# Kernel tuning notes

Measured on AMD Instinct MI355X. Metric: run time of the kernel, lower is better.

The kernel has to match this reference:

```python
import jax, jax.numpy as jnp
import numpy as np

HEADS = 16
DIM_HEAD = 64
SCALE = DIM_HEAD ** -0.5


def setup_inputs() -> dict:
    key = jax.random.key(0)
    k1, k2, k3 = jax.random.split(key, 3)
    B, N, C = 2, 2048, 1024
    inner = HEADS * DIM_HEAD  # 1024
    x = jax.random.normal(k1, (B, N, C), dtype=jnp.float32)
    w_qkv = jax.random.normal(k2, (C, 3 * inner), dtype=jnp.float32) * (C ** -0.5)
    w_proj = jax.random.normal(k3, (inner, C), dtype=jnp.float32) * (inner ** -0.5)
    b_proj = jnp.zeros((C,), dtype=jnp.float32)
    return {"x": x, "w_qkv": w_qkv, "w_proj": w_proj, "b_proj": b_proj}


def reference(x, w_qkv, w_proj, b_proj):
    B, N, C = x.shape
    qkv = x @ w_qkv  # [B, N, 3*inner]
    qkv = qkv.reshape(B, N, 3, HEADS, DIM_HEAD)
    qkv = jnp.transpose(qkv, (2, 0, 3, 1, 4))  # [3, B, H, N, D]
    q, k, v = qkv[0], qkv[1], qkv[2]
    q = q * SCALE
    attn = jnp.einsum('bhnd,bhmd->bhnm', q, k)  # [B, H, N, N]
    attn = jax.nn.softmax(attn, axis=-1)
    out = jnp.einsum('bhnm,bhmd->bhnd', attn, v)  # [B, H, N, D]
    out = jnp.transpose(out, (0, 2, 1, 3)).reshape(B, N, HEADS * DIM_HEAD)
    return out @ w_proj + b_proj
```

## Files before the change

kernel.cpp:

```cpp
#include <hip/hip_runtime.h>
#include <hip/hip_bf16.h>
#include <cstdint>
#include <cstddef>

static constexpr int BATCH = 2;
static constexpr int SEQ   = 2048;
static constexpr int CDIM  = 1024;
static constexpr int ROWS  = BATCH * SEQ;
static constexpr int QKVN  = 3 * CDIM;
static constexpr int QKN   = 2 * CDIM;

typedef short bf16x8 __attribute__((ext_vector_type(8)));
typedef short bf16x4 __attribute__((ext_vector_type(4)));
typedef float f32x4  __attribute__((ext_vector_type(4)));

__device__ inline short f2bf(float f) {
    union { float f; unsigned u; } v; v.f = f;
    unsigned u = v.u;
    u += 0x7fffu + ((u >> 16) & 1u);
    return (short)(u >> 16);
}

__device__ inline unsigned pk_bf16(float a, float b) {
#if __has_builtin(__builtin_amdgcn_cvt_pk_bf16_f32)
    auto r = __builtin_amdgcn_cvt_pk_bf16_f32(a, b);
    return __builtin_bit_cast(unsigned, r);
#else
    union { float f; unsigned u; } ua, ub;
    ua.f = a; ub.f = b;
    unsigned xa = ua.u + 0x7fffu + ((ua.u >> 16) & 1u);
    unsigned xb = ub.u + 0x7fffu + ((ub.u >> 16) & 1u);
    return __builtin_amdgcn_perm(xb, xa, 0x07060302);
#endif
}

__device__ inline void glds16(const short* g, short* l) {
    __builtin_amdgcn_global_load_lds(
        (const __attribute__((address_space(1))) void*)g,
        (__attribute__((address_space(3))) void*)l, 16, 0, 0);
}

__device__ inline f32x4 mfma16_bf16(bf16x4 a, bf16x4 b, f32x4 c) {
#if __has_builtin(__builtin_amdgcn_mfma_f32_16x16x16bf16_1k)
    return __builtin_amdgcn_mfma_f32_16x16x16bf16_1k(a, b, c, 0, 0, 0);
#else
    asm("v_mfma_f32_16x16x16_bf16 %0, %1, %2, %0" : "+v"(c) : "v"(a), "v"(b));
    return c;
#endif
}

__global__ __launch_bounds__(256) void prep(const float* __restrict__ x,
                                            const float* __restrict__ wqkv,
                                            const float* __restrict__ wproj,
                                            short* __restrict__ x_bf,
                                            short* __restrict__ wqkvT,
                                            short* __restrict__ wprojT,
                                            float smul) {
    __shared__ float tile[32][33];
    const int bid = blockIdx.x, t = threadIdx.x;
    if (bid < 4096) {
        int i = bid * 256 + t;
        float4 f = ((const float4*)x)[i];
        uint2 o;
        o.x = pk_bf16(f.x, f.y);
        o.y = pk_bf16(f.z, f.w);
        ((uint2*)x_bf)[i] = o;
        return;
    }
    const float* in; short* out; int C, r0, c0; float scale; int srows;
    if (bid < 7168) {
        int b2 = bid - 4096;
        in = wqkv; out = wqkvT; C = QKVN;
        c0 = (b2 % 96) * 32; r0 = (b2 / 96) * 32;
        scale = smul; srows = 1024;
    } else {
        int b3 = bid - 7168;
        in = wproj; out = wprojT; C = CDIM;
        c0 = (b3 & 31) * 32; r0 = (b3 >> 5) * 32;
        scale = 1.0f; srows = 0;
    }
    int tx = t & 31, ty = t >> 5;
    #pragma unroll
    for (int i = 0; i < 4; i++)
        tile[ty + i * 8][tx] = in[(size_t)(r0 + ty + i * 8) * C + c0 + tx];
    __syncthreads();
    #pragma unroll
    for (int i = 0; i < 4; i++) {
        int orow = c0 + ty + i * 8;
        float sc = (orow < srows) ? scale : 1.0f;
        out[(size_t)orow * CDIM + r0 + tx] = f2bf(tile[tx][ty + i * 8] * sc);
    }
}

template<int BF16OUT, int MT>
__device__ __forceinline__ void gemm_core(const short* __restrict__ A,
                                          const short* __restrict__ Bt,
                                          void* __restrict__ C,
                                          const float* __restrict__ bias,
                                          int N, int K, int m0, int n0,
                                          short* As, short* Bs) {
    constexpr int AF = MT / 32;
    const int t = threadIdx.x, wave = t >> 6, lane = t & 63;
    const int l15 = lane & 15, quad = lane >> 4;
    const int wr = wave >> 1, wc = wave & 1;

    f32x4 acc[AF][4] = {};

    const short* gA = A  + (size_t)(m0 + wave * (MT / 4) + (lane >> 2)) * K + (lane & 3) * 8;
    const short* gB = Bt + (size_t)(n0 + wave * 32 + (lane >> 2)) * K + (lane & 3) * 8;
    short* lA = &As[wave * (MT / 4) * 32];
    short* lB = &Bs[wave * 32 * 32];

    for (int k0 = 0; k0 < K; k0 += 32) {
        glds16(gA + k0, lA);
        if constexpr (MT == 128) glds16(gA + 16 * K + k0, lA + 512);
        glds16(gB + k0,          lB);
        glds16(gB + 16 * K + k0, lB + 512);
        __syncthreads();

        bf16x8 af[AF], bf[4];
        #pragma unroll
        for (int i = 0; i < AF; i++)
            af[i] = *(const bf16x8*)&As[(wr * (MT / 2) + i * 16 + l15) * 32 + quad * 8];
        #pragma unroll
        for (int j = 0; j < 4; j++)
            bf[j] = *(const bf16x8*)&Bs[(wc * 64 + j * 16 + l15) * 32 + quad * 8];
        #pragma unroll
        for (int i = 0; i < AF; i++)
            #pragma unroll
            for (int j = 0; j < 4; j++)
                acc[i][j] = __builtin_amdgcn_mfma_f32_16x16x32_bf16(af[i], bf[j], acc[i][j], 0, 0, 0);
        __syncthreads();
    }

    #pragma unroll
    for (int i = 0; i < AF; i++) {
        #pragma unroll
        for (int j = 0; j < 4; j++) {
            #pragma unroll
            for (int r = 0; r < 4; r++) {
                int row = m0 + wr * (MT / 2) + i * 16 + quad * 4 + r;
                int col = n0 + wc * 64 + j * 16 + l15;
                float v = acc[i][j][r];
                if (BF16OUT) ((short*)C)[(size_t)row * N + col] = f2bf(v);
                else         ((float*)C)[(size_t)row * N + col] = v + bias[col];
            }
        }
    }
}

__global__ __launch_bounds__(256) void gemm_qk_v(const short* __restrict__ x_bf,
                                                 const short* __restrict__ wqkvT,
                                                 short* __restrict__ qk,
                                                 short* __restrict__ vT) {
    __shared__ __align__(16) short As[128 * 32];
    __shared__ __align__(16) short Bs[128 * 32];
    const int bid = blockIdx.x;
    if (bid < 512) {
        gemm_core<1, 128>(x_bf, wqkvT, qk, nullptr, QKN, CDIM,
                          (bid >> 4) * 128, (bid & 15) * 128, As, Bs);
    } else {
        int b2 = bid - 512;
        gemm_core<1, 64>(wqkvT + (size_t)QKN * CDIM, x_bf, vT, nullptr, ROWS, CDIM,
                         (b2 >> 5) * 64, (b2 & 31) * 128, As, Bs);
    }
}

__global__ __launch_bounds__(256) void gemm_proj(const short* __restrict__ A,
                                                 const short* __restrict__ Bt,
                                                 float* __restrict__ C,
                                                 const float* __restrict__ bias) {
    __shared__ __align__(16) short As[64 * 32];
    __shared__ __align__(16) short Bs[128 * 32];
    gemm_core<0, 64>(A, Bt, C, bias, CDIM, CDIM,
                     blockIdx.y * 64, blockIdx.x * 128, As, Bs);
}

static constexpr int KBUF  = 2 * 128 * 32;
static constexpr int VOFF  = 2 * KBUF;
static constexpr int LDV   = 136;
static constexpr int VBUF  = 64 * LDV;
static constexpr int SMEM_SH = VOFF + 2 * VBUF;

__global__ __launch_bounds__(256) void attn_kernel(const short* __restrict__ qk,
                                                   const short* __restrict__ vTg,
                                                   short* __restrict__ attn_out) {
    __shared__ __align__(16) short smem[SMEM_SH];

    const int t = threadIdx.x, wave = t >> 6, lane = t & 63;
    const int l15 = lane & 15, quad = lane >> 4;
    const int bh = blockIdx.y, b = bh >> 4, h = bh & 15;
    const int q0 = blockIdx.x * 128;
    const size_t baseQ = (size_t)(b * SEQ) * QKN + h * 64;

    const size_t qoff0 = baseQ + (size_t)(q0 + wave * 32 + l15) * QKN + quad * 8;
    const size_t qoff1 = qoff0 + (size_t)16 * QKN;
    bf16x8 qf00 = *(const bf16x8*)&qk[qoff0];
    bf16x8 qf01 = *(const bf16x8*)&qk[qoff0 + 32];
    bf16x8 qf10 = *(const bf16x8*)&qk[qoff1];
    bf16x8 qf11 = *(const bf16x8*)&qk[qoff1 + 32];

    const short* gK = qk + baseQ + 1024
                    + (size_t)(wave * 32 + (lane >> 2)) * QKN + (lane & 3) * 8;
    const short* gV = vTg + (size_t)(h * 64) * ROWS + b * SEQ;
    const int vd = t >> 2, vc = t & 3;

    const bf16x4 ones = { (short)0x3F80, (short)0x3F80, (short)0x3F80, (short)0x3F80 };

    f32x4 ot0[4] = {}, ot1[4] = {};
    f32x4 ol0 = {}, ol1 = {};

    glds16(gK,                 smem + wave * 1024);
    glds16(gK + 16 * QKN,      smem + wave * 1024 + 512);
    glds16(gK + 32,            smem + 4096 + wave * 1024);
    glds16(gK + 16 * QKN + 32, smem + 4096 + wave * 1024 + 512);
    #pragma unroll
    for (int c = 0; c < 4; c++) {
        int4 v = *(const int4*)&gV[(size_t)vd * ROWS + vc * 8 + c * 32];
        *(int4*)&smem[VOFF + vd * LDV + vc * 8 + c * 32] = v;
    }

    for (int j = 0; j < SEQ / 128; j++) {
        const int cur = j & 1, nxt = cur ^ 1;
        __syncthreads();

        int4 va[4];
        if (j < SEQ / 128 - 1) {
            const size_t jadd = (size_t)(j + 1) * 128 * QKN;
            short* kb = smem + nxt * KBUF + wave * 1024;
            glds16(gK + jadd,                 kb);
            glds16(gK + jadd + 16 * QKN,      kb + 512);
            glds16(gK + jadd + 32,            kb + 4096);
            glds16(gK + jadd + 16 * QKN + 32, kb + 4096 + 512);
            #pragma unroll
            for (int c = 0; c < 4; c++)
                va[c] = *(const int4*)&gV[(size_t)vd * ROWS + (j + 1) * 128 + vc * 8 + c * 32];
        }

        const short* Kb0 = smem + cur * KBUF;
        const short* Kb1 = Kb0 + 4096;
        const short* Vb  = smem + VOFF + cur * VBUF;

        #pragma unroll
        for (int sub = 0; sub < 8; sub++) {
            bf16x8 kf0 = *(const bf16x8*)&Kb0[(sub * 16 + l15) * 32 + quad * 8];
            bf16x8 kf1 = *(const bf16x8*)&Kb1[(sub * 16 + l15) * 32 + quad * 8];
            f32x4 a0 = {}, a1 = {};
            a0 = __builtin_amdgcn_mfma_f32_16x16x32_bf16(kf0, qf00, a0, 0, 0, 0);
            a0 = __builtin_amdgcn_mfma_f32_16x16x32_bf16(kf1, qf01, a0, 0, 0, 0);
            a1 = __builtin_amdgcn_mfma_f32_16x16x32_bf16(kf0, qf10, a1, 0, 0, 0);
            a1 = __builtin_amdgcn_mfma_f32_16x16x32_bf16(kf1, qf11, a1, 0, 0, 0);
            union { unsigned u[2]; bf16x4 v; } pu0, pu1;
            pu0.u[0] = pk_bf16(__builtin_amdgcn_exp2f(a0[0]), __builtin_amdgcn_exp2f(a0[1]));
            pu0.u[1] = pk_bf16(__builtin_amdgcn_exp2f(a0[2]), __builtin_amdgcn_exp2f(a0[3]));
            pu1.u[0] = pk_bf16(__builtin_amdgcn_exp2f(a1[0]), __builtin_amdgcn_exp2f(a1[1]));
            pu1.u[1] = pk_bf16(__builtin_amdgcn_exp2f(a1[2]), __builtin_amdgcn_exp2f(a1[3]));
            ol0 = mfma16_bf16(ones, pu0.v, ol0);
            ol1 = mfma16_bf16(ones, pu1.v, ol1);
            #pragma unroll
            for (int d = 0; d < 4; d++) {
                bf16x4 vf = *(const bf16x4*)&Vb[(d * 16 + l15) * LDV + sub * 16 + quad * 4];
                ot0[d] = mfma16_bf16(vf, pu0.v, ot0[d]);
                ot1[d] = mfma16_bf16(vf, pu1.v, ot1[d]);
            }
        }

        if (j < SEQ / 128 - 1) {
            #pragma unroll
            for (int c = 0; c < 4; c++)
                *(int4*)&smem[VOFF + nxt * VBUF + vd * LDV + vc * 8 + c * 32] = va[c];
        }
    }

    __syncthreads();
    float inv0 = 1.0f / ol0[0], inv1 = 1.0f / ol1[0];
    #pragma unroll
    for (int d = 0; d < 4; d++) {
        int r0 = (wave * 32 + l15) * 72 + d * 16 + quad * 4;
        *(unsigned*)&smem[r0]     = pk_bf16(ot0[d][0] * inv0, ot0[d][1] * inv0);
        *(unsigned*)&smem[r0 + 2] = pk_bf16(ot0[d][2] * inv0, ot0[d][3] * inv0);
        int r1 = (wave * 32 + 16 + l15) * 72 + d * 16 + quad * 4;
        *(unsigned*)&smem[r1]     = pk_bf16(ot1[d][0] * inv1, ot1[d][1] * inv1);
        *(unsigned*)&smem[r1 + 2] = pk_bf16(ot1[d][2] * inv1, ot1[d][3] * inv1);
    }
    __syncthreads();
    {
        int row = t >> 1, c2 = t & 1;
        #pragma unroll
        for (int p = 0; p < 4; p++) {
            int ch = c2 * 4 + p;
            int4 v = *(const int4*)&smem[row * 72 + ch * 8];
            *(int4*)&attn_out[(size_t)(b * SEQ + q0 + row) * CDIM + h * 64 + ch * 8] = v;
        }
    }
}

extern "C" void kernel_launch(void* const* d_in, const int* in_sizes, int n_in,
                              void* d_out, int out_size, void* d_ws, size_t ws_size,
                              hipStream_t stream) {
    const float* x      = (const float*)d_in[0];
    const float* w_qkv  = (const float*)d_in[1];
    const float* w_proj = (const float*)d_in[2];
    const float* b_proj = (const float*)d_in[3];
    float* out = (float*)d_out;

    char* ws = (char*)d_ws;
    short* x_bf    = (short*)(ws);
    short* wqkvT   = (short*)(ws + 8388608);
    short* wprojT  = (short*)(ws + 14680064);
    short* qk_bf   = (short*)(ws + 16777216);
    short* vTg     = (short*)(ws + 33554432);
    short* attn_bf = (short*)(ws + 41943040);

    const float SMUL = 0.125f * 1.44269504088896340736f;

    prep<<<8192, 256, 0, stream>>>(x, w_qkv, w_proj, x_bf, wqkvT, wprojT, SMUL);

    gemm_qk_v<<<1024, 256, 0, stream>>>(x_bf, wqkvT, qk_bf, vTg);

    attn_kernel<<<dim3(SEQ / 128, BATCH * 16), 256, 0, stream>>>(qk_bf, vTg, attn_bf);

    gemm_proj<<<dim3(CDIM / 128, ROWS / 64), 256, 0, stream>>>(attn_bf, wprojT, out, b_proj);
}
```

Measured before the change: 211.7 us.

## Split attention KV tile across two wave groups with LDS reduction

Doubles the attention block to 512 threads. Two groups of four waves each process half of every 128-key tile for the same 128 queries, then combine their partial output and row-sum accumulators through shared memory before normalising. The aim is more waves per CU to hide latency in the grid of 512 blocks, and shorter per-wave dependency chains. In exchange it adds a final cross-group reduction with extra syncs and LDS traffic, and uses more registers per block, which may limit occupancy.

Result: faster. 193.2 us (-8.7%).

```diff
diff --git a/kernel.cpp b/kernel.cpp
--- a/kernel.cpp
+++ b/kernel.cpp
@@ -182,18 +182,19 @@
 static constexpr int VBUF  = 64 * LDV;
 static constexpr int SMEM_SH = VOFF + 2 * VBUF;
 
-__global__ __launch_bounds__(256) void attn_kernel(const short* __restrict__ qk,
+__global__ __launch_bounds__(512) void attn_kernel(const short* __restrict__ qk,
                                                    const short* __restrict__ vTg,
                                                    short* __restrict__ attn_out) {
     __shared__ __align__(16) short smem[SMEM_SH];
 
     const int t = threadIdx.x, wave = t >> 6, lane = t & 63;
     const int l15 = lane & 15, quad = lane >> 4;
+    const int g = wave >> 2, wl = wave & 3;
     const int bh = blockIdx.y, b = bh >> 4, h = bh & 15;
     const int q0 = blockIdx.x * 128;
     const size_t baseQ = (size_t)(b * SEQ) * QKN + h * 64;
 
-    const size_t qoff0 = baseQ + (size_t)(q0 + wave * 32 + l15) * QKN + quad * 8;
+    const size_t qoff0 = baseQ + (size_t)(q0 + wl * 32 + l15) * QKN + quad * 8;
     const size_t qoff1 = qoff0 + (size_t)16 * QKN;
     bf16x8 qf00 = *(const bf16x8*)&qk[qoff0];
     bf16x8 qf01 = *(const bf16x8*)&qk[qoff0 + 32];
@@ -201,40 +202,36 @@
     bf16x8 qf11 = *(const bf16x8*)&qk[qoff1 + 32];
 
     const short* gK = qk + baseQ + 1024
-                    + (size_t)(wave * 32 + (lane >> 2)) * QKN + (lane & 3) * 8;
+                    + (size_t)(wave * 16 + (lane >> 2)) * QKN + (lane & 3) * 8;
     const short* gV = vTg + (size_t)(h * 64) * ROWS + b * SEQ;
-    const int vd = t >> 2, vc = t & 3;
+    const int vd = t >> 3, vc = t & 7;
 
     const bf16x4 ones = { (short)0x3F80, (short)0x3F80, (short)0x3F80, (short)0x3F80 };
 
     f32x4 ot0[4] = {}, ot1[4] = {};
     f32x4 ol0 = {}, ol1 = {};
 
-    glds16(gK,                 smem + wave * 1024);
-    glds16(gK + 16 * QKN,      smem + wave * 1024 + 512);
-    glds16(gK + 32,            smem + 4096 + wave * 1024);
-    glds16(gK + 16 * QKN + 32, smem + 4096 + wave * 1024 + 512);
-    #pragma unroll
-    for (int c = 0; c < 4; c++) {
-        int4 v = *(const int4*)&gV[(size_t)vd * ROWS + vc * 8 + c * 32];
-        *(int4*)&smem[VOFF + vd * LDV + vc * 8 + c * 32] = v;
+    glds16(gK,      smem + wave * 512);
+    glds16(gK + 32, smem + 4096 + wave * 512);
+    {
+        int4 va = *(const int4*)&gV[(size_t)vd * ROWS + vc * 8];
+        int4 vb = *(const int4*)&gV[(size_t)vd * ROWS + 64 + vc * 8];
+        *(int4*)&smem[VOFF + vd * LDV + vc * 8]      = va;
+        *(int4*)&smem[VOFF + vd * LDV + 64 + vc * 8] = vb;
     }
 
     for (int j = 0; j < SEQ / 128; j++) {
         const int cur = j & 1, nxt = cur ^ 1;
         __syncthreads();
 
-        int4 va[4];
+        int4 va, vb;
         if (j < SEQ / 128 - 1) {
             const size_t jadd = (size_t)(j + 1) * 128 * QKN;
-            short* kb = smem + nxt * KBUF + wave * 1024;
-            glds16(gK + jadd,                 kb);
-            glds16(gK + jadd + 16 * QKN,      kb + 512);
-            glds16(gK + jadd + 32,            kb + 4096);
-            glds16(gK + jadd + 16 * QKN + 32, kb + 4096 + 512);
-            #pragma unroll
-            for (int c = 0; c < 4; c++)
-                va[c] = *(const int4*)&gV[(size_t)vd * ROWS + (j + 1) * 128 + vc * 8 + c * 32];
+            short* kb = smem + nxt * KBUF + wave * 512;
+            glds16(gK + jadd,      kb);
+            glds16(gK + jadd + 32, kb + 4096);
+            va = *(const int4*)&gV[(size_t)vd * ROWS + (j + 1) * 128 + vc * 8];
+            vb = *(const int4*)&gV[(size_t)vd * ROWS + (j + 1) * 128 + 64 + vc * 8];
         }
 
         const short* Kb0 = smem + cur * KBUF;
@@ -242,9 +239,10 @@
         const short* Vb  = smem + VOFF + cur * VBUF;
 
         #pragma unroll
-        for (int sub = 0; sub < 8; sub++) {
-            bf16x8 kf0 = *(const bf16x8*)&Kb0[(sub * 16 + l15) * 32 + quad * 8];
-            bf16x8 kf1 = *(const bf16x8*)&Kb1[(sub * 16 + l15) * 32 + quad * 8];
+        for (int sub = 0; sub < 4; sub++) {
+            const int gsub = g * 4 + sub;
+            bf16x8 kf0 = *(const bf16x8*)&Kb0[(gsub * 16 + l15) * 32 + quad * 8];
+            bf16x8 kf1 = *(const bf16x8*)&Kb1[(gsub * 16 + l15) * 32 + quad * 8];
             f32x4 a0 = {}, a1 = {};
             a0 = __builtin_amdgcn_mfma_f32_16x16x32_bf16(kf0, qf00, a0, 0, 0, 0);
             a0 = __builtin_amdgcn_mfma_f32_16x16x32_bf16(kf1, qf01, a0, 0, 0, 0);
@@ -259,37 +257,66 @@
             ol1 = mfma16_bf16(ones, pu1.v, ol1);
             #pragma unroll
             for (int d = 0; d < 4; d++) {
-                bf16x4 vf = *(const bf16x4*)&Vb[(d * 16 + l15) * LDV + sub * 16 + quad * 4];
+                bf16x4 vf = *(const bf16x4*)&Vb[(d * 16 + l15) * LDV + gsub * 16 + quad * 4];
                 ot0[d] = mfma16_bf16(vf, pu0.v, ot0[d]);
                 ot1[d] = mfma16_bf16(vf, pu1.v, ot1[d]);
             }
         }
 
         if (j < SEQ / 128 - 1) {
+            *(int4*)&smem[VOFF + nxt * VBUF + vd * LDV + vc * 8]      = va;
+            *(int4*)&smem[VOFF + nxt * VBUF + vd * LDV + 64 + vc * 8] = vb;
+        }
+    }
+
+    __syncthreads();
+    float* pf   = (float*)smem;
+    float* lbuf = (float*)smem + 128 * 68;
+    short* tr   = smem + 18432;
+
+    if (g == 1) {
+        #pragma unroll
+        for (int d = 0; d < 4; d++) {
             #pragma unroll
-            for (int c = 0; c < 4; c++)
-                *(int4*)&smem[VOFF + nxt * VBUF + vd * LDV + vc * 8 + c * 32] = va[c];
-        }
-    }
-
+            for (int r = 0; r < 4; r++) {
+                pf[(wl * 32 + l15) * 68      + d * 16 + quad * 4 + r] = ot0[d][r];
+                pf[(wl * 32 + 16 + l15) * 68 + d * 16 + quad * 4 + r] = ot1[d][r];
+            }
+        }
+        lbuf[wl * 32 + l15]      = ol0[0];
+        lbuf[wl * 32 + 16 + l15] = ol1[0];
+    }
     __syncthreads();
-    float inv0 = 1.0f / ol0[0], inv1 = 1.0f / ol1[0];
-    #pragma unroll
-    for (int d = 0; d < 4; d++) {
-        int r0 = (wave * 32 + l15) * 72 + d * 16 + quad * 4;
-        *(unsigned*)&smem[r0]     = pk_bf16(ot0[d][0] * inv0, ot0[d][1] * inv0);
-        *(unsigned*)&smem[r0 + 2] = pk_bf16(ot0[d][2] * inv0, ot0[d][3] * inv0);
-        int r1 = (wave * 32 + 16 + l15) * 72 + d * 16 + quad * 4;
-        *(unsigned*)&smem[r1]     = pk_bf16(ot1[d][0] * inv1, ot1[d][1] * inv1);
-        *(unsigned*)&smem[r1 + 2] = pk_bf16(ot1[d][2] * inv1, ot1[d][3] * inv1);
+    if (g == 0) {
+        float inv0 = 1.0f / (ol0[0] + lbuf[wl * 32 + l15]);
+        float inv1 = 1.0f / (ol1[0] + lbuf[wl * 32 + 16 + l15]);
+        #pragma unroll
+        for (int d = 0; d < 4; d++) {
+            int pb0 = (wl * 32 + l15) * 68      + d * 16 + quad * 4;
+            int pb1 = (wl * 32 + 16 + l15) * 68 + d * 16 + quad * 4;
+            float c00 = (ot0[d][0] + pf[pb0 + 0]) * inv0;
+            float c01 = (ot0[d][1] + pf[pb0 + 1]) * inv0;
+            float c02 = (ot0[d][2] + pf[pb0 + 2]) * inv0;
+            float c03 = (ot0[d][3] + pf[pb0 + 3]) * inv0;
+            float c10 = (ot1[d][0] + pf[pb1 + 0]) * inv1;
+            float c11 = (ot1[d][1] + pf[pb1 + 1]) * inv1;
+            float c12 = (ot1[d][2] + pf[pb1 + 2]) * inv1;
+            float c13 = (ot1[d][3] + pf[pb1 + 3]) * inv1;
+            int o0 = (wl * 32 + l15) * 72 + d * 16 + quad * 4;
+            int o1 = (wl * 32 + 16 + l15) * 72 + d * 16 + quad * 4;
+            *(unsigned*)&tr[o0]     = pk_bf16(c00, c01);
+            *(unsigned*)&tr[o0 + 2] = pk_bf16(c02, c03);
+            *(unsigned*)&tr[o1]     = pk_bf16(c10, c11);
+            *(unsigned*)&tr[o1 + 2] = pk_bf16(c12, c13);
+        }
     }
     __syncthreads();
     {
-        int row = t >> 1, c2 = t & 1;
-        #pragma unroll
-        for (int p = 0; p < 4; p++) {
-            int ch = c2 * 4 + p;
-            int4 v = *(const int4*)&smem[row * 72 + ch * 8];
+        int row = t >> 2, c4 = t & 3;
+        #pragma unroll
+        for (int p = 0; p < 2; p++) {
+            int ch = c4 * 2 + p;
+            int4 v = *(const int4*)&tr[row * 72 + ch * 8];
             *(int4*)&attn_out[(size_t)(b * SEQ + q0 + row) * CDIM + h * 64 + ch * 8] = v;
         }
     }
@@ -318,7 +345,7 @@
 
     gemm_qk_v<<<1024, 256, 0, stream>>>(x_bf, wqkvT, qk_bf, vTg);
 
-    attn_kernel<<<dim3(SEQ / 128, BATCH * 16), 256, 0, stream>>>(qk_bf, vTg, attn_bf);
+    attn_kernel<<<dim3(SEQ / 128, BATCH * 16), 512, 0, stream>>>(qk_bf, vTg, attn_bf);
 
     gemm_proj<<<dim3(CDIM / 128, ROWS / 64), 256, 0, stream>>>(attn_bf, wprojT, out, b_proj);
 }
```
